# Optimization experiments

Hardware: AMD Instinct MI355X
Metric: run time of the kernel (lower is better)

## Reference

```python
import jax, jax.numpy as jnp
import numpy as np
from jax import lax

B, T, D = 2, 512, 64   # batch, temporal length, input_dim
H = 64                 # hidden_dims
OUT = 64               # output_dim
REL = 2 * D            # relation_dim = input_dim * 2 (until=True: max & min interval pooling)


def _interval_pool(f, op):
    """f: [B,T,D] -> r: [B,T,T,D] with r[:, i, j] = op-reduction of f[:, i..j] for i <= j.
    Entries with i > j are filled with f[:, i] (degenerate interval); they are never
    read because the downstream backward pooling only reduces over j >= i."""
    Tn = f.shape[1]
    idx = jnp.arange(Tn)

    def step(col, j):
        # col[:, i] holds reduce(f[:, i..j-1]) for i <= j-1, and f[:, i] otherwise
        new = op(col, f[:, j][:, None, :])                      # extend interval to j
        new = jnp.where((idx <= j)[None, :, None], new, f)      # reset i > j rows
        return new, new

    _, cols = lax.scan(step, f, jnp.arange(Tn))  # [T(j), B, T(i), D]
    return jnp.transpose(cols, (1, 2, 0, 3))     # [B, T(i), T(j), D]


def _backward_max_pool(s):
    """s: [B,T,T,C] -> out[:, i] = max_{j >= i} s[:, i, j]  (the 'broadcast' backward pool)."""
    Tn = s.shape[1]
    mask = jnp.arange(Tn)[:, None] <= jnp.arange(Tn)[None, :]   # i <= j
    neg = jnp.asarray(-1e9, s.dtype)
    return jnp.max(jnp.where(mask[None, :, :, None], s, neg), axis=2)


def setup_inputs() -> dict:
    key = jax.random.key(0)
    ks = jax.random.split(key, 7)
    f = jax.random.normal(ks[0], (B, T, D), dtype=jnp.float32)
    # step_linears per __init__: current_dim starts at REL, then hidden_dims
    dims = [(REL + REL, H), (H + REL, H), (H + REL, OUT)]
    params = {}
    for i, (din, dout) in enumerate(dims):
        params[f"W{i}"] = jax.random.normal(ks[1 + 2 * i], (din, dout), jnp.float32) / np.sqrt(din)
        params[f"b{i}"] = jnp.zeros((dout,), jnp.float32)
    return {"f": f, **params}


def reference(f, W0, b0, W1, b1, W2, b2):
    Tn = f.shape[1]
    # until=True: concat max- and min-interval pooling -> [B,T,T,2D]
    r = jnp.concatenate([_interval_pool(f, jnp.maximum),
                         _interval_pool(f, jnp.minimum)], axis=-1)
    current = r[:, :, Tn - 1]  # [B, T, REL] : reductions over suffix intervals [i, T-1]
    for W, b in ((W0, b0), (W1, b1), (W2, b2)):
        # jactorch.add_dim(current, 1, t): broadcast current (indexed by j) over new i axis
        bcast = jnp.broadcast_to(current[:, None, :, :],
                                 (f.shape[0], Tn, Tn, current.shape[-1]))
        li = jnp.concatenate([bcast, r], axis=-1)                 # [B,T,T,C+REL]
        h = jax.nn.sigmoid(jnp.einsum('bijc,co->bijo', li, W) + b)  # MLPLogic, no hidden layers
        current = _backward_max_pool(h)                           # [B,T,out]
    return current
```

## Files before the change

kernel.cpp:

```cpp
#include <hip/hip_runtime.h>
#include <hip/hip_bf16.h>
#include <math.h>

#define B_ 2
#define T_ 512
#define D_ 64
#define NBLK_PER_B 1088

typedef __attribute__((ext_vector_type(8))) short bf16x8;
typedef __attribute__((ext_vector_type(8))) unsigned short u16x8;
typedef __attribute__((ext_vector_type(4))) float f32x4;

static __device__ __forceinline__ unsigned short f2bf(float v) {
    __hip_bfloat16 h = __float2bfloat16(v);
    return *reinterpret_cast<unsigned short*>(&h);
}
static __device__ __forceinline__ float bf2f(unsigned short u) {
    return __uint_as_float(((unsigned)u) << 16);
}
static __device__ __forceinline__ unsigned short maxbits(unsigned short a, unsigned short b) {
    float m = fmaxf(bf2f(a), bf2f(b));
    return (unsigned short)(__float_as_uint(m) >> 16);
}
static __device__ __forceinline__ unsigned short minbits(unsigned short a, unsigned short b) {
    float m = fminf(bf2f(a), bf2f(b));
    return (unsigned short)(__float_as_uint(m) >> 16);
}

__global__ __launch_bounds__(512) void prep_kernel(
    const float* __restrict__ f,
    const float* __restrict__ W0, const float* __restrict__ W1, const float* __restrict__ W2,
    unsigned short* __restrict__ tmax, unsigned short* __restrict__ tmin,
    unsigned short* __restrict__ wf,
    unsigned short* __restrict__ cur0bf, unsigned short* __restrict__ intra,
    float* __restrict__ z0, float* __restrict__ z1, float* __restrict__ z2) {

    __shared__ unsigned short lmax[512][16];
    __shared__ unsigned short lmin[512][16];

    const int blk = blockIdx.x;
    const int tid = threadIdx.x;

    if (blk < 8) {
        const int b = blk & 1;
        const int c0 = (blk >> 1) * 16;
        const int t = tid;

        u16x8 mx[2], mn[2];
#pragma unroll
        for (int h = 0; h < 2; ++h) {
            const float* fp = &f[((size_t)(b * T_ + t) << 6) + c0 + h * 8];
#pragma unroll
            for (int e = 0; e < 8; ++e) {
                unsigned short u = f2bf(fp[e]);
                mx[h][e] = u; mn[h][e] = u;
            }
            size_t base = ((size_t)(b * T_ + t) << 6) + c0 + h * 8;
            *reinterpret_cast<u16x8*>(&tmax[base]) = mx[h];
            *reinterpret_cast<u16x8*>(&tmin[base]) = mn[h];
        }
        for (int k = 1; k <= 9; ++k) {
            *reinterpret_cast<u16x8*>(&lmax[t][0]) = mx[0];
            *reinterpret_cast<u16x8*>(&lmax[t][8]) = mx[1];
            *reinterpret_cast<u16x8*>(&lmin[t][0]) = mn[0];
            *reinterpret_cast<u16x8*>(&lmin[t][8]) = mn[1];
            __syncthreads();
            int t2 = t + (1 << (k - 1));
            if (t2 > T_ - 1) t2 = T_ - 1;
            u16x8 qx0 = *reinterpret_cast<const u16x8*>(&lmax[t2][0]);
            u16x8 qx1 = *reinterpret_cast<const u16x8*>(&lmax[t2][8]);
            u16x8 qn0 = *reinterpret_cast<const u16x8*>(&lmin[t2][0]);
            u16x8 qn1 = *reinterpret_cast<const u16x8*>(&lmin[t2][8]);
#pragma unroll
            for (int e = 0; e < 8; ++e) {
                mx[0][e] = maxbits(mx[0][e], qx0[e]);
                mx[1][e] = maxbits(mx[1][e], qx1[e]);
                mn[0][e] = minbits(mn[0][e], qn0[e]);
                mn[1][e] = minbits(mn[1][e], qn1[e]);
            }
            size_t base = ((size_t)((k * B_ + b) * T_ + t) << 6) + c0;
            *reinterpret_cast<u16x8*>(&tmax[base]) = mx[0];
            *reinterpret_cast<u16x8*>(&tmax[base + 8]) = mx[1];
            *reinterpret_cast<u16x8*>(&tmin[base]) = mn[0];
            *reinterpret_cast<u16x8*>(&tmin[base + 8]) = mn[1];
            __syncthreads();
        }
    } else if (blk < 11) {
        const int layer = blk - 8;
        const float* W = (layer == 0) ? W0 : ((layer == 1) ? W1 : W2);
        const int FRS = (layer == 0) ? 32 : 24;
        const int l = tid & 63;
        for (int fr = tid >> 6; fr < FRS; fr += 8) {
            int kt = fr >> 2, nt = fr & 3;
#pragma unroll
            for (int e = 0; e < 8; ++e) {
                int row = kt * 32 + ((l >> 4) << 3) + e;
                int col = nt * 16 + (l & 15);
                wf[((size_t)(layer * 32 + fr) * 64 + l) * 8 + e] = f2bf(W[row * 64 + col]);
            }
        }
    } else if (blk < 139) {
        const int x = blk - 11;
        const int c = x & 63, b = x >> 6;
        const int t = tid;
        float* smax = reinterpret_cast<float*>(lmax);
        float* smin = reinterpret_cast<float*>(lmin);
        float v = f[((size_t)(b * T_ + t) << 6) + c];
        smax[t] = v; smin[t] = v;
        __syncthreads();
        for (int off = 1; off < 512; off <<= 1) {
            float a = (t + off < 512) ? smax[t + off] : -1e30f;
            float m = (t + off < 512) ? smin[t + off] : 1e30f;
            __syncthreads();
            smax[t] = fmaxf(smax[t], a);
            smin[t] = fminf(smin[t], m);
            __syncthreads();
        }
        cur0bf[((size_t)(b * T_ + t) << 7) + c] = f2bf(smax[t]);
        cur0bf[((size_t)(b * T_ + t) << 7) + 64 + c] = f2bf(smin[t]);
    } else if (blk < 171) {
        const int x = blk - 139;
        const int jt = x & 15, b = x >> 4;
        const int jj = tid >> 4, c8 = tid & 15;
        const bool ismin = c8 >= 8;
        unsigned short (*sc)[128] = reinterpret_cast<unsigned short (*)[128]>(lmax);

        const float* fp = &f[((size_t)(b * T_ + jt * 32 + jj) << 6) + (c8 & 7) * 8];
        u16x8 r;
#pragma unroll
        for (int e = 0; e < 8; ++e) r[e] = f2bf(fp[e]);

#pragma unroll
        for (int off = 1; off < 32; off <<= 1) {
            *reinterpret_cast<u16x8*>(&sc[jj][c8 * 8]) = r;
            __syncthreads();
            if (jj >= off) {
                u16x8 q = *reinterpret_cast<const u16x8*>(&sc[jj - off][c8 * 8]);
#pragma unroll
                for (int e = 0; e < 8; ++e)
                    r[e] = ismin ? minbits(r[e], q[e]) : maxbits(r[e], q[e]);
            }
            __syncthreads();
        }
        *reinterpret_cast<u16x8*>(&intra[((size_t)((b * 16 + jt) * 32 + jj) << 7) + c8 * 8]) = r;
    } else {
        int fi = (blk - 171) * 512 + tid;
        float4 z = {0.f, 0.f, 0.f, 0.f};
        if (fi < 16384)       reinterpret_cast<float4*>(z0)[fi] = z;
        else if (fi < 32768)  reinterpret_cast<float4*>(z1)[fi - 16384] = z;
        else                  reinterpret_cast<float4*>(z2)[fi - 32768] = z;
    }
}

template <int C, bool FROM_TAB>
__global__ __launch_bounds__(256) void pair_kernel(
    const unsigned short* __restrict__ tabmax,
    const unsigned short* __restrict__ tabmin,
    const unsigned short* __restrict__ cur0bf,
    const unsigned short* __restrict__ intra,
    const float* __restrict__ curprev,
    const unsigned short* __restrict__ wf,
    const float* __restrict__ bias,
    float* __restrict__ out) {

    constexpr int KTC = C / 32;
    constexpr int KT = KTC + 4;
    constexpr int CP = (C == 128) ? 136 : 72;

    int m = blockIdx.x;
    int b = 0;
    if (m >= NBLK_PER_B) { b = 1; m -= NBLK_PER_B; }
    int jt = 0;
    while (m >= 4 * (jt + 1) * (jt + 2)) ++jt;
    const int it = m - 4 * jt * (jt + 1);
    const bool diag = (it >= 8 * jt);
    const int i0 = it * 4, j0 = jt * 32;

    const int tid = threadIdx.x;
    const int l = tid & 63, w = tid >> 6;
    const int lg = l >> 4, li = l & 15;

    __shared__ unsigned short curl[32][CP];
    __shared__ unsigned short intr[32][136];
    __shared__ unsigned short pref[4][136];

    if (FROM_TAB) {
#pragma unroll
        for (int q = 0; q < 2; ++q) {
            int chn = q * 256 + tid;
            int jj = chn >> 4, c8 = chn & 15;
            u16x8 v = *reinterpret_cast<const u16x8*>(
                &cur0bf[((size_t)(b * T_ + j0 + jj) << 7) + c8 * 8]);
            *reinterpret_cast<u16x8*>(&curl[jj][c8 * 8]) = v;
        }
    } else {
        int jj = tid >> 3, c8 = tid & 7;
        const float* cp = &curprev[((size_t)(b * T_ + j0 + jj) << 6) + c8 * 8];
        float4 v0 = *reinterpret_cast<const float4*>(cp);
        float4 v1 = *reinterpret_cast<const float4*>(cp + 4);
        u16x8 r;
        r[0] = f2bf(v0.x); r[1] = f2bf(v0.y); r[2] = f2bf(v0.z); r[3] = f2bf(v0.w);
        r[4] = f2bf(v1.x); r[5] = f2bf(v1.y); r[6] = f2bf(v1.z); r[7] = f2bf(v1.w);
        *reinterpret_cast<u16x8*>(&curl[jj][c8 * 8]) = r;
    }

    if (!diag) {
#pragma unroll
        for (int q = 0; q < 2; ++q) {
            int chn = q * 256 + tid;
            int jj = chn >> 4, c8 = chn & 15;
            u16x8 v = *reinterpret_cast<const u16x8*>(
                &intra[((size_t)((b * 16 + jt) * 32 + jj) << 7) + c8 * 8]);
            *reinterpret_cast<u16x8*>(&intr[jj][c8 * 8]) = v;
        }
        if (tid < 64) {
            int isel = tid >> 4, c8 = tid & 15;
            int i = i0 + isel;
            int len = j0 - i;
            int kk = 31 - __clz(len);
            int t2 = j0 - (1 << kk);
            const unsigned short* tab = (c8 < 8) ? tabmax : tabmin;
            int cc = (c8 & 7) * 8;
            u16x8 va = *reinterpret_cast<const u16x8*>(&tab[(((size_t)(kk * B_ + b) * T_ + i) << 6) + cc]);
            u16x8 vb = *reinterpret_cast<const u16x8*>(&tab[(((size_t)(kk * B_ + b) * T_ + t2) << 6) + cc]);
            u16x8 r;
#pragma unroll
            for (int e = 0; e < 8; ++e)
                r[e] = (c8 < 8) ? maxbits(va[e], vb[e]) : minbits(va[e], vb[e]);
            *reinterpret_cast<u16x8*>(&pref[isel][c8 * 8]) = r;
        }
    }
    __syncthreads();

    f32x4 acc[2][4];
#pragma unroll
    for (int s = 0; s < 2; ++s)
#pragma unroll
        for (int nt = 0; nt < 4; ++nt) acc[s][nt] = (f32x4){0.f, 0.f, 0.f, 0.f};

    const int pi = i0 + w;

#pragma unroll
    for (int kt = 0; kt < KT; ++kt) {
        bf16x8 bfr[4];
#pragma unroll
        for (int nt = 0; nt < 4; ++nt)
            bfr[nt] = *reinterpret_cast<const bf16x8*>(&wf[(size_t)((kt * 4 + nt) * 64 + l) * 8]);

#pragma unroll
        for (int s = 0; s < 2; ++s) {
            const int pjj = 16 * s + li;
            bf16x8 av;
            if (kt < KTC) {
                av = *reinterpret_cast<const bf16x8*>(&curl[pjj][kt * 32 + lg * 8]);
            } else {
                const int krt = kt - KTC;
                const int c8 = krt * 4 + lg;
                if (!diag) {
                    u16x8 iv = *reinterpret_cast<const u16x8*>(&intr[pjj][c8 * 8]);
                    u16x8 pv = *reinterpret_cast<const u16x8*>(&pref[w][c8 * 8]);
#pragma unroll
                    for (int e = 0; e < 8; ++e)
                        av[e] = (short)((c8 < 8) ? maxbits(iv[e], pv[e]) : minbits(iv[e], pv[e]));
                } else {
                    const int pj = j0 + pjj;
                    const int je = (pj < pi) ? pi : pj;
                    const int len = je - pi + 1;
                    const int kk = 31 - __clz(len);
                    const int t2 = je + 1 - (1 << kk);
                    const unsigned short* tab = (c8 < 8) ? tabmax : tabmin;
                    const int cc = (c8 & 7) * 8;
                    u16x8 va = *reinterpret_cast<const u16x8*>(&tab[(((size_t)(kk * B_ + b) * T_ + pi) << 6) + cc]);
                    u16x8 vb = *reinterpret_cast<const u16x8*>(&tab[(((size_t)(kk * B_ + b) * T_ + t2) << 6) + cc]);
#pragma unroll
                    for (int e = 0; e < 8; ++e)
                        av[e] = (short)((c8 < 8) ? maxbits(va[e], vb[e]) : minbits(va[e], vb[e]));
                }
            }
#pragma unroll
            for (int nt = 0; nt < 4; ++nt)
                acc[s][nt] = __builtin_amdgcn_mfma_f32_16x16x32_bf16(av, bfr[nt], acc[s][nt], 0, 0, 0);
        }
    }

#pragma unroll
    for (int nt = 0; nt < 4; ++nt) {
        float vm = -1e9f;
#pragma unroll
        for (int s = 0; s < 2; ++s)
#pragma unroll
            for (int r = 0; r < 4; ++r) {
                int jj = 16 * s + lg * 4 + r;
                if (j0 + jj >= pi) vm = fmaxf(vm, acc[s][nt][r]);
            }
        vm = fmaxf(vm, __shfl_xor(vm, 16));
        vm = fmaxf(vm, __shfl_xor(vm, 32));
        if (l < 16) {
            int o = nt * 16 + li;
            float h = 1.0f / (1.0f + __expf(-(vm + bias[o])));
            atomicMax((int*)out + (((size_t)(b * T_ + pi) << 6) + o), __float_as_int(h));
        }
    }
}

extern "C" void kernel_launch(void* const* d_in, const int* in_sizes, int n_in,
                              void* d_out, int out_size, void* d_ws, size_t ws_size,
                              hipStream_t stream) {
    const float* f  = (const float*)d_in[0];
    const float* W0 = (const float*)d_in[1];
    const float* b0 = (const float*)d_in[2];
    const float* W1 = (const float*)d_in[3];
    const float* b1 = (const float*)d_in[4];
    const float* W2 = (const float*)d_in[5];
    const float* b2 = (const float*)d_in[6];
    float* outp = (float*)d_out;

    unsigned short* tabmax = (unsigned short*)d_ws;
    unsigned short* tabmin = tabmax + 10 * B_ * T_ * 64;
    unsigned short* wf     = tabmin + 10 * B_ * T_ * 64;
    unsigned short* cur0bf = wf + 3 * 32 * 64 * 8;
    unsigned short* intra  = cur0bf + B_ * T_ * 128;
    float* cur1 = (float*)(intra + B_ * 16 * 32 * 128);
    float* cur2 = cur1 + B_ * T_ * 64;

    prep_kernel<<<dim3(267), dim3(512), 0, stream>>>(f, W0, W1, W2,
                                                     tabmax, tabmin, wf,
                                                     cur0bf, intra,
                                                     cur1, cur2, outp);

    const dim3 pgrid(B_ * NBLK_PER_B);
    pair_kernel<128, true ><<<pgrid, dim3(256), 0, stream>>>(tabmax, tabmin, cur0bf, intra,
                                                             nullptr, wf + 0 * 32 * 64 * 8, b0, cur1);
    pair_kernel<64,  false><<<pgrid, dim3(256), 0, stream>>>(tabmax, tabmin, cur0bf, intra,
                                                             cur1, wf + 1 * 32 * 64 * 8, b1, cur2);
    pair_kernel<64,  false><<<pgrid, dim3(256), 0, stream>>>(tabmax, tabmin, cur0bf, intra,
                                                             cur2, wf + 2 * 32 * 64 * 8, b2, outp);
}
```

Baseline: 83.53 us.

## Make pair blocks persistent over j-tiles with register-held weights and double-buffered staging

Each pair_kernel block now owns one 4-row i tile and walks half of its j tiles (split by parity), instead of launching one block per (i,j) tile pair. This cuts the grid from 2176 to 512 blocks. Weight fragments are loaded into registers once per block, and the per-tile inputs (cur, intra, prefix) are double-buffered in shared memory, with the next tile's global loads issued before the current tile's MFMAs. The row max is accumulated in registers across tiles, so each block issues far fewer atomics. In exchange, register pressure rises under launch_bounds(256,2), the work per block is uneven across i tiles, and there is less parallelism to hide latency.

```diff
diff --git a/kernel.cpp b/kernel.cpp
--- a/kernel.cpp
+++ b/kernel.cpp
@@ -5,7 +5,6 @@
 #define B_ 2
 #define T_ 512
 #define D_ 64
-#define NBLK_PER_B 1088
 
 typedef __attribute__((ext_vector_type(8))) short bf16x8;
 typedef __attribute__((ext_vector_type(8))) unsigned short u16x8;
@@ -153,7 +152,7 @@
 }
 
 template <int C, bool FROM_TAB>
-__global__ __launch_bounds__(256) void pair_kernel(
+__global__ __launch_bounds__(256, 2) void pair_kernel(
     const unsigned short* __restrict__ tabmax,
     const unsigned short* __restrict__ tabmin,
     const unsigned short* __restrict__ cur0bf,
@@ -167,138 +166,215 @@
     constexpr int KT = KTC + 4;
     constexpr int CP = (C == 128) ? 136 : 72;
 
-    int m = blockIdx.x;
-    int b = 0;
-    if (m >= NBLK_PER_B) { b = 1; m -= NBLK_PER_B; }
-    int jt = 0;
-    while (m >= 4 * (jt + 1) * (jt + 2)) ++jt;
-    const int it = m - 4 * jt * (jt + 1);
-    const bool diag = (it >= 8 * jt);
-    const int i0 = it * 4, j0 = jt * 32;
+    const int bx = blockIdx.x;
+    const int b = bx >> 8;
+    const int rem = bx & 255;
+    const int it = rem >> 1;
+    const int h = rem & 1;
+    const int i0 = it * 4;
+    const int jt0 = it >> 3;
+    const int start = jt0 + (h ? 1 : 2);
+    if (h && start > 15) return;
 
     const int tid = threadIdx.x;
     const int l = tid & 63, w = tid >> 6;
     const int lg = l >> 4, li = l & 15;
-
-    __shared__ unsigned short curl[32][CP];
-    __shared__ unsigned short intr[32][136];
-    __shared__ unsigned short pref[4][136];
-
-    if (FROM_TAB) {
-#pragma unroll
-        for (int q = 0; q < 2; ++q) {
-            int chn = q * 256 + tid;
-            int jj = chn >> 4, c8 = chn & 15;
-            u16x8 v = *reinterpret_cast<const u16x8*>(
-                &cur0bf[((size_t)(b * T_ + j0 + jj) << 7) + c8 * 8]);
-            *reinterpret_cast<u16x8*>(&curl[jj][c8 * 8]) = v;
+    const int pi = i0 + w;
+    const int jj_lo = tid >> 4, c8s = tid & 15;
+
+    __shared__ unsigned short curl[2][32][CP];
+    __shared__ unsigned short intr[2][32][136];
+    __shared__ unsigned short pref[2][4][136];
+
+    bf16x8 wfr[KT][4];
+#pragma unroll
+    for (int kt = 0; kt < KT; ++kt)
+#pragma unroll
+        for (int nt = 0; nt < 4; ++nt)
+            wfr[kt][nt] = *reinterpret_cast<const bf16x8*>(&wf[(size_t)((kt * 4 + nt) * 64 + l) * 8]);
+
+    float vmax[4] = {-1e9f, -1e9f, -1e9f, -1e9f};
+
+    u16x8 Rcur0, Rcur1;
+    float4 Rf0, Rf1;
+    u16x8 Rint0, Rint1;
+    u16x8 Rpva, Rpvb;
+
+    auto issue = [&](int jtn) {
+        const int j0n = jtn * 32;
+        if (FROM_TAB) {
+            const unsigned short* cb = &cur0bf[((size_t)(b * T_ + j0n) << 7)];
+            Rcur0 = *reinterpret_cast<const u16x8*>(&cb[(jj_lo << 7) + c8s * 8]);
+            Rcur1 = *reinterpret_cast<const u16x8*>(&cb[((jj_lo + 16) << 7) + c8s * 8]);
+        } else {
+            const float* cp = &curprev[((size_t)(b * T_ + j0n + (tid >> 3)) << 6) + (tid & 7) * 8];
+            Rf0 = *reinterpret_cast<const float4*>(cp);
+            Rf1 = *reinterpret_cast<const float4*>(cp + 4);
+        }
+        const unsigned short* ib = &intra[((size_t)((b * 16 + jtn) * 32) << 7)];
+        Rint0 = *reinterpret_cast<const u16x8*>(&ib[(jj_lo << 7) + c8s * 8]);
+        Rint1 = *reinterpret_cast<const u16x8*>(&ib[((jj_lo + 16) << 7) + c8s * 8]);
+        if (l < 16) {
+            int len = j0n - pi;
+            int kk = 31 - __clz(len);
+            int t2 = j0n - (1 << kk);
+            const unsigned short* tab = (li < 8) ? tabmax : tabmin;
+            int cc = (li & 7) * 8;
+            Rpva = *reinterpret_cast<const u16x8*>(&tab[(((size_t)(kk * B_ + b) * T_ + pi) << 6) + cc]);
+            Rpvb = *reinterpret_cast<const u16x8*>(&tab[(((size_t)(kk * B_ + b) * T_ + t2) << 6) + cc]);
+        }
+    };
+
+    auto wstage = [&](int p) {
+        if (FROM_TAB) {
+            *reinterpret_cast<u16x8*>(&curl[p][jj_lo][c8s * 8]) = Rcur0;
+            *reinterpret_cast<u16x8*>(&curl[p][jj_lo + 16][c8s * 8]) = Rcur1;
+        } else {
+            u16x8 r;
+            r[0] = f2bf(Rf0.x); r[1] = f2bf(Rf0.y); r[2] = f2bf(Rf0.z); r[3] = f2bf(Rf0.w);
+            r[4] = f2bf(Rf1.x); r[5] = f2bf(Rf1.y); r[6] = f2bf(Rf1.z); r[7] = f2bf(Rf1.w);
+            *reinterpret_cast<u16x8*>(&curl[p][tid >> 3][(tid & 7) * 8]) = r;
+        }
+        *reinterpret_cast<u16x8*>(&intr[p][jj_lo][c8s * 8]) = Rint0;
+        *reinterpret_cast<u16x8*>(&intr[p][jj_lo + 16][c8s * 8]) = Rint1;
+        if (l < 16) {
+            u16x8 r;
+#pragma unroll
+            for (int e = 0; e < 8; ++e)
+                r[e] = (li < 8) ? maxbits(Rpva[e], Rpvb[e]) : minbits(Rpva[e], Rpvb[e]);
+            *reinterpret_cast<u16x8*>(&pref[p][w][li * 8]) = r;
+        }
+    };
+
+    auto compute = [&](int p) {
+        f32x4 acc[2][4];
+#pragma unroll
+        for (int s = 0; s < 2; ++s)
+#pragma unroll
+            for (int nt = 0; nt < 4; ++nt) acc[s][nt] = (f32x4){0.f, 0.f, 0.f, 0.f};
+
+        u16x8 pv[4];
+#pragma unroll
+        for (int krt = 0; krt < 4; ++krt)
+            pv[krt] = *reinterpret_cast<const u16x8*>(&pref[p][w][(krt * 4 + lg) * 8]);
+
+#pragma unroll
+        for (int kt = 0; kt < KT; ++kt) {
+#pragma unroll
+            for (int s = 0; s < 2; ++s) {
+                const int pjj = 16 * s + li;
+                bf16x8 av;
+                if (kt < KTC) {
+                    av = *reinterpret_cast<const bf16x8*>(&curl[p][pjj][kt * 32 + lg * 8]);
+                } else {
+                    const int krt = kt - KTC;
+                    u16x8 iv = *reinterpret_cast<const u16x8*>(&intr[p][pjj][(krt * 4 + lg) * 8]);
+                    if (krt < 2) {
+#pragma unroll
+                        for (int e = 0; e < 8; ++e) av[e] = (short)maxbits(iv[e], pv[krt][e]);
+                    } else {
+#pragma unroll
+                        for (int e = 0; e < 8; ++e) av[e] = (short)minbits(iv[e], pv[krt][e]);
+                    }
+                }
+#pragma unroll
+                for (int nt = 0; nt < 4; ++nt)
+                    acc[s][nt] = __builtin_amdgcn_mfma_f32_16x16x32_bf16(av, wfr[kt][nt], acc[s][nt], 0, 0, 0);
+            }
+        }
+#pragma unroll
+        for (int nt = 0; nt < 4; ++nt)
+#pragma unroll
+            for (int s = 0; s < 2; ++s)
+#pragma unroll
+                for (int r = 0; r < 4; ++r)
+                    vmax[nt] = fmaxf(vmax[nt], acc[s][nt][r]);
+    };
+
+    if (!h) {
+        if (start <= 15) issue(start);
+        {
+            const int j0 = jt0 * 32;
+            f32x4 acc[2][4];
+#pragma unroll
+            for (int s = 0; s < 2; ++s)
+#pragma unroll
+                for (int nt = 0; nt < 4; ++nt) acc[s][nt] = (f32x4){0.f, 0.f, 0.f, 0.f};
+
+#pragma unroll
+            for (int kt = 0; kt < KT; ++kt) {
+#pragma unroll
+                for (int s = 0; s < 2; ++s) {
+                    const int pjj = 16 * s + li;
+                    bf16x8 av;
+                    if (kt < KTC) {
+                        if (FROM_TAB) {
+                            av = *reinterpret_cast<const bf16x8*>(
+                                &cur0bf[((size_t)(b * T_ + j0 + pjj) << 7) + kt * 32 + lg * 8]);
+                        } else {
+                            const float* cp = &curprev[((size_t)(b * T_ + j0 + pjj) << 6) + kt * 32 + lg * 8];
+                            float4 v0 = *reinterpret_cast<const float4*>(cp);
+                            float4 v1 = *reinterpret_cast<const float4*>(cp + 4);
+                            av[0] = f2bf(v0.x); av[1] = f2bf(v0.y); av[2] = f2bf(v0.z); av[3] = f2bf(v0.w);
+                            av[4] = f2bf(v1.x); av[5] = f2bf(v1.y); av[6] = f2bf(v1.z); av[7] = f2bf(v1.w);
+                        }
+                    } else {
+                        const int krt = kt - KTC;
+                        const int c8 = krt * 4 + lg;
+                        const int pj = j0 + pjj;
+                        const int je = (pj < pi) ? pi : pj;
+                        const int len = je - pi + 1;
+                        const int kk = 31 - __clz(len);
+                        const int t2 = je + 1 - (1 << kk);
+                        const unsigned short* tab = (krt < 2) ? tabmax : tabmin;
+                        const int cc = (c8 & 7) * 8;
+                        u16x8 va = *reinterpret_cast<const u16x8*>(&tab[(((size_t)(kk * B_ + b) * T_ + pi) << 6) + cc]);
+                        u16x8 vb = *reinterpret_cast<const u16x8*>(&tab[(((size_t)(kk * B_ + b) * T_ + t2) << 6) + cc]);
+                        if (krt < 2) {
+#pragma unroll
+                            for (int e = 0; e < 8; ++e) av[e] = (short)maxbits(va[e], vb[e]);
+                        } else {
+#pragma unroll
+                            for (int e = 0; e < 8; ++e) av[e] = (short)minbits(va[e], vb[e]);
+                        }
+                    }
+#pragma unroll
+                    for (int nt = 0; nt < 4; ++nt)
+                        acc[s][nt] = __builtin_amdgcn_mfma_f32_16x16x32_bf16(av, wfr[kt][nt], acc[s][nt], 0, 0, 0);
+                }
+            }
+#pragma unroll
+            for (int nt = 0; nt < 4; ++nt)
+#pragma unroll
+                for (int s = 0; s < 2; ++s)
+#pragma unroll
+                    for (int r = 0; r < 4; ++r) {
+                        int jj = 16 * s + lg * 4 + r;
+                        if (j0 + jj >= pi) vmax[nt] = fmaxf(vmax[nt], acc[s][nt][r]);
+                    }
         }
     } else {
-        int jj = tid >> 3, c8 = tid & 7;
-        const float* cp = &curprev[((size_t)(b * T_ + j0 + jj) << 6) + c8 * 8];
-        float4 v0 = *reinterpret_cast<const float4*>(cp);
-        float4 v1 = *reinterpret_cast<const float4*>(cp + 4);
-        u16x8 r;
-        r[0] = f2bf(v0.x); r[1] = f2bf(v0.y); r[2] = f2bf(v0.z); r[3] = f2bf(v0.w);
-        r[4] = f2bf(v1.x); r[5] = f2bf(v1.y); r[6] = f2bf(v1.z); r[7] = f2bf(v1.w);
-        *reinterpret_cast<u16x8*>(&curl[jj][c8 * 8]) = r;
+        issue(start);
     }
 
-    if (!diag) {
-#pragma unroll
-        for (int q = 0; q < 2; ++q) {
-            int chn = q * 256 + tid;
-            int jj = chn >> 4, c8 = chn & 15;
-            u16x8 v = *reinterpret_cast<const u16x8*>(
-                &intra[((size_t)((b * 16 + jt) * 32 + jj) << 7) + c8 * 8]);
-            *reinterpret_cast<u16x8*>(&intr[jj][c8 * 8]) = v;
-        }
-        if (tid < 64) {
-            int isel = tid >> 4, c8 = tid & 15;
-            int i = i0 + isel;
-            int len = j0 - i;
-            int kk = 31 - __clz(len);
-            int t2 = j0 - (1 << kk);
-            const unsigned short* tab = (c8 < 8) ? tabmax : tabmin;
-            int cc = (c8 & 7) * 8;
-            u16x8 va = *reinterpret_cast<const u16x8*>(&tab[(((size_t)(kk * B_ + b) * T_ + i) << 6) + cc]);
-            u16x8 vb = *reinterpret_cast<const u16x8*>(&tab[(((size_t)(kk * B_ + b) * T_ + t2) << 6) + cc]);
-            u16x8 r;
-#pragma unroll
-            for (int e = 0; e < 8; ++e)
-                r[e] = (c8 < 8) ? maxbits(va[e], vb[e]) : minbits(va[e], vb[e]);
-            *reinterpret_cast<u16x8*>(&pref[isel][c8 * 8]) = r;
-        }
+    int p = 0;
+    for (int jt = start; jt <= 15; jt += 2) {
+        wstage(p);
+        __syncthreads();
+        if (jt + 2 <= 15) issue(jt + 2);
+        compute(p);
+        p ^= 1;
     }
-    __syncthreads();
-
-    f32x4 acc[2][4];
-#pragma unroll
-    for (int s = 0; s < 2; ++s)
-#pragma unroll
-        for (int nt = 0; nt < 4; ++nt) acc[s][nt] = (f32x4){0.f, 0.f, 0.f, 0.f};
-
-    const int pi = i0 + w;
-
-#pragma unroll
-    for (int kt = 0; kt < KT; ++kt) {
-        bf16x8 bfr[4];
-#pragma unroll
-        for (int nt = 0; nt < 4; ++nt)
-            bfr[nt] = *reinterpret_cast<const bf16x8*>(&wf[(size_t)((kt * 4 + nt) * 64 + l) * 8]);
-
-#pragma unroll
-        for (int s = 0; s < 2; ++s) {
-            const int pjj = 16 * s + li;
-            bf16x8 av;
-            if (kt < KTC) {
-                av = *reinterpret_cast<const bf16x8*>(&curl[pjj][kt * 32 + lg * 8]);
-            } else {
-                const int krt = kt - KTC;
-                const int c8 = krt * 4 + lg;
-                if (!diag) {
-                    u16x8 iv = *reinterpret_cast<const u16x8*>(&intr[pjj][c8 * 8]);
-                    u16x8 pv = *reinterpret_cast<const u16x8*>(&pref[w][c8 * 8]);
-#pragma unroll
-                    for (int e = 0; e < 8; ++e)
-                        av[e] = (short)((c8 < 8) ? maxbits(iv[e], pv[e]) : minbits(iv[e], pv[e]));
-                } else {
-                    const int pj = j0 + pjj;
-                    const int je = (pj < pi) ? pi : pj;
-                    const int len = je - pi + 1;
-                    const int kk = 31 - __clz(len);
-                    const int t2 = je + 1 - (1 << kk);
-                    const unsigned short* tab = (c8 < 8) ? tabmax : tabmin;
-                    const int cc = (c8 & 7) * 8;
-                    u16x8 va = *reinterpret_cast<const u16x8*>(&tab[(((size_t)(kk * B_ + b) * T_ + pi) << 6) + cc]);
-                    u16x8 vb = *reinterpret_cast<const u16x8*>(&tab[(((size_t)(kk * B_ + b) * T_ + t2) << 6) + cc]);
-#pragma unroll
-                    for (int e = 0; e < 8; ++e)
-                        av[e] = (short)((c8 < 8) ? maxbits(va[e], vb[e]) : minbits(va[e], vb[e]));
-                }
-            }
-#pragma unroll
-            for (int nt = 0; nt < 4; ++nt)
-                acc[s][nt] = __builtin_amdgcn_mfma_f32_16x16x32_bf16(av, bfr[nt], acc[s][nt], 0, 0, 0);
-        }
-    }
 
 #pragma unroll
     for (int nt = 0; nt < 4; ++nt) {
-        float vm = -1e9f;
-#pragma unroll
-        for (int s = 0; s < 2; ++s)
-#pragma unroll
-            for (int r = 0; r < 4; ++r) {
-                int jj = 16 * s + lg * 4 + r;
-                if (j0 + jj >= pi) vm = fmaxf(vm, acc[s][nt][r]);
-            }
+        float vm = vmax[nt];
         vm = fmaxf(vm, __shfl_xor(vm, 16));
         vm = fmaxf(vm, __shfl_xor(vm, 32));
         if (l < 16) {
             int o = nt * 16 + li;
-            float h = 1.0f / (1.0f + __expf(-(vm + bias[o])));
-            atomicMax((int*)out + (((size_t)(b * T_ + pi) << 6) + o), __float_as_int(h));
+            float hh = 1.0f / (1.0f + __expf(-(vm + bias[o])));
+            atomicMax((int*)out + (((size_t)(b * T_ + pi) << 6) + o), __float_as_int(hh));
         }
     }
 }
@@ -328,7 +404,7 @@
                                                      cur0bf, intra,
                                                      cur1, cur2, outp);
 
-    const dim3 pgrid(B_ * NBLK_PER_B);
+    const dim3 pgrid(B_ * 128 * 2);
     pair_kernel<128, true ><<<pgrid, dim3(256), 0, stream>>>(tabmax, tabmin, cur0bf, intra,
                                                              nullptr, wf + 0 * 32 * 64 * 8, b0, cur1);
     pair_kernel<64,  false><<<pgrid, dim3(256), 0, stream>>>(tabmax, tabmin, cur0bf, intra,
```

Result: slower. 97.91 us (+17.2%).

## Load pair-kernel operands directly from global memory, dropping LDS staging and barrier

Applied to the files above, without the earlier changes.

Removes the shared-memory staging of the current-feature tile, the intra-block table and the prefix rows, along with the block-wide __syncthreads. Each wave now reads its MFMA A-operands straight from global memory (the L2/L1 caches) and computes its own prefix vectors in registers. It also hoists the per-lane sparse-table indices for diagonal tiles out of the k loop and resolves the max/min choice at compile time. The cost is redundant global loads across the 4 waves, since each row is now fetched once per wave, plus extra register pressure from the pv array.

```diff
diff --git a/kernel.cpp b/kernel.cpp
--- a/kernel.cpp
+++ b/kernel.cpp
@@ -165,7 +165,6 @@
 
     constexpr int KTC = C / 32;
     constexpr int KT = KTC + 4;
-    constexpr int CP = (C == 128) ? 136 : 72;
 
     int m = blockIdx.x;
     int b = 0;
@@ -179,107 +178,97 @@
     const int tid = threadIdx.x;
     const int l = tid & 63, w = tid >> 6;
     const int lg = l >> 4, li = l & 15;
-
-    __shared__ unsigned short curl[32][CP];
-    __shared__ unsigned short intr[32][136];
-    __shared__ unsigned short pref[4][136];
-
-    if (FROM_TAB) {
-#pragma unroll
-        for (int q = 0; q < 2; ++q) {
-            int chn = q * 256 + tid;
-            int jj = chn >> 4, c8 = chn & 15;
-            u16x8 v = *reinterpret_cast<const u16x8*>(
-                &cur0bf[((size_t)(b * T_ + j0 + jj) << 7) + c8 * 8]);
-            *reinterpret_cast<u16x8*>(&curl[jj][c8 * 8]) = v;
+    const int pi = i0 + w;
+
+    u16x8 pv[4];
+    int kk_s[2], t2_s[2], je_s[2];
+    if (!diag) {
+        const int len = j0 - pi;
+        const int kk = 31 - __clz(len);
+        const int t2 = j0 - (1 << kk);
+#pragma unroll
+        for (int krt = 0; krt < 4; ++krt) {
+            const int c8 = krt * 4 + lg;
+            const unsigned short* tab = (c8 < 8) ? tabmax : tabmin;
+            const int cc = (c8 & 7) * 8;
+            u16x8 va = *reinterpret_cast<const u16x8*>(&tab[(((size_t)(kk * B_ + b) * T_ + pi) << 6) + cc]);
+            u16x8 vb = *reinterpret_cast<const u16x8*>(&tab[(((size_t)(kk * B_ + b) * T_ + t2) << 6) + cc]);
+#pragma unroll
+            for (int e = 0; e < 8; ++e)
+                pv[krt][e] = (c8 < 8) ? maxbits(va[e], vb[e]) : minbits(va[e], vb[e]);
         }
     } else {
-        int jj = tid >> 3, c8 = tid & 7;
-        const float* cp = &curprev[((size_t)(b * T_ + j0 + jj) << 6) + c8 * 8];
-        float4 v0 = *reinterpret_cast<const float4*>(cp);
-        float4 v1 = *reinterpret_cast<const float4*>(cp + 4);
-        u16x8 r;
-        r[0] = f2bf(v0.x); r[1] = f2bf(v0.y); r[2] = f2bf(v0.z); r[3] = f2bf(v0.w);
-        r[4] = f2bf(v1.x); r[5] = f2bf(v1.y); r[6] = f2bf(v1.z); r[7] = f2bf(v1.w);
-        *reinterpret_cast<u16x8*>(&curl[jj][c8 * 8]) = r;
+#pragma unroll
+        for (int s = 0; s < 2; ++s) {
+            const int pj = j0 + 16 * s + li;
+            const int je = (pj < pi) ? pi : pj;
+            const int len = je - pi + 1;
+            kk_s[s] = 31 - __clz(len);
+            t2_s[s] = je + 1 - (1 << kk_s[s]);
+            je_s[s] = je;
+        }
     }
 
-    if (!diag) {
-#pragma unroll
-        for (int q = 0; q < 2; ++q) {
-            int chn = q * 256 + tid;
-            int jj = chn >> 4, c8 = chn & 15;
-            u16x8 v = *reinterpret_cast<const u16x8*>(
-                &intra[((size_t)((b * 16 + jt) * 32 + jj) << 7) + c8 * 8]);
-            *reinterpret_cast<u16x8*>(&intr[jj][c8 * 8]) = v;
-        }
-        if (tid < 64) {
-            int isel = tid >> 4, c8 = tid & 15;
-            int i = i0 + isel;
-            int len = j0 - i;
-            int kk = 31 - __clz(len);
-            int t2 = j0 - (1 << kk);
-            const unsigned short* tab = (c8 < 8) ? tabmax : tabmin;
-            int cc = (c8 & 7) * 8;
-            u16x8 va = *reinterpret_cast<const u16x8*>(&tab[(((size_t)(kk * B_ + b) * T_ + i) << 6) + cc]);
-            u16x8 vb = *reinterpret_cast<const u16x8*>(&tab[(((size_t)(kk * B_ + b) * T_ + t2) << 6) + cc]);
-            u16x8 r;
-#pragma unroll
-            for (int e = 0; e < 8; ++e)
-                r[e] = (c8 < 8) ? maxbits(va[e], vb[e]) : minbits(va[e], vb[e]);
-            *reinterpret_cast<u16x8*>(&pref[isel][c8 * 8]) = r;
-        }
-    }
-    __syncthreads();
-
     f32x4 acc[2][4];
 #pragma unroll
     for (int s = 0; s < 2; ++s)
 #pragma unroll
         for (int nt = 0; nt < 4; ++nt) acc[s][nt] = (f32x4){0.f, 0.f, 0.f, 0.f};
 
-    const int pi = i0 + w;
-
 #pragma unroll
     for (int kt = 0; kt < KT; ++kt) {
-        bf16x8 bfr[4];
+        bf16x8 wfr[4];
 #pragma unroll
         for (int nt = 0; nt < 4; ++nt)
-            bfr[nt] = *reinterpret_cast<const bf16x8*>(&wf[(size_t)((kt * 4 + nt) * 64 + l) * 8]);
+            wfr[nt] = *reinterpret_cast<const bf16x8*>(&wf[(size_t)((kt * 4 + nt) * 64 + l) * 8]);
 
 #pragma unroll
         for (int s = 0; s < 2; ++s) {
             const int pjj = 16 * s + li;
+            const int pj = j0 + pjj;
             bf16x8 av;
             if (kt < KTC) {
-                av = *reinterpret_cast<const bf16x8*>(&curl[pjj][kt * 32 + lg * 8]);
+                if (FROM_TAB) {
+                    av = *reinterpret_cast<const bf16x8*>(
+                        &cur0bf[((size_t)(b * T_ + pj) << 7) + kt * 32 + lg * 8]);
+                } else {
+                    const float* cp = &curprev[((size_t)(b * T_ + pj) << 6) + kt * 32 + lg * 8];
+                    float4 v0 = *reinterpret_cast<const float4*>(cp);
+                    float4 v1 = *reinterpret_cast<const float4*>(cp + 4);
+                    av[0] = f2bf(v0.x); av[1] = f2bf(v0.y); av[2] = f2bf(v0.z); av[3] = f2bf(v0.w);
+                    av[4] = f2bf(v1.x); av[5] = f2bf(v1.y); av[6] = f2bf(v1.z); av[7] = f2bf(v1.w);
+                }
             } else {
                 const int krt = kt - KTC;
-                const int c8 = krt * 4 + lg;
                 if (!diag) {
-                    u16x8 iv = *reinterpret_cast<const u16x8*>(&intr[pjj][c8 * 8]);
-                    u16x8 pv = *reinterpret_cast<const u16x8*>(&pref[w][c8 * 8]);
-#pragma unroll
-                    for (int e = 0; e < 8; ++e)
-                        av[e] = (short)((c8 < 8) ? maxbits(iv[e], pv[e]) : minbits(iv[e], pv[e]));
+                    u16x8 iv = *reinterpret_cast<const u16x8*>(
+                        &intra[((size_t)((b * 16 + jt) * 32 + pjj) << 7) + (krt * 4 + lg) * 8]);
+                    if (krt < 2) {
+#pragma unroll
+                        for (int e = 0; e < 8; ++e) av[e] = (short)maxbits(iv[e], pv[krt][e]);
+                    } else {
+#pragma unroll
+                        for (int e = 0; e < 8; ++e) av[e] = (short)minbits(iv[e], pv[krt][e]);
+                    }
                 } else {
-                    const int pj = j0 + pjj;
-                    const int je = (pj < pi) ? pi : pj;
-                    const int len = je - pi + 1;
-                    const int kk = 31 - __clz(len);
-                    const int t2 = je + 1 - (1 << kk);
-                    const unsigned short* tab = (c8 < 8) ? tabmax : tabmin;
+                    const int c8 = krt * 4 + lg;
+                    const unsigned short* tab = (krt < 2) ? tabmax : tabmin;
                     const int cc = (c8 & 7) * 8;
+                    const int kk = kk_s[s], t2 = t2_s[s];
                     u16x8 va = *reinterpret_cast<const u16x8*>(&tab[(((size_t)(kk * B_ + b) * T_ + pi) << 6) + cc]);
                     u16x8 vb = *reinterpret_cast<const u16x8*>(&tab[(((size_t)(kk * B_ + b) * T_ + t2) << 6) + cc]);
-#pragma unroll
-                    for (int e = 0; e < 8; ++e)
-                        av[e] = (short)((c8 < 8) ? maxbits(va[e], vb[e]) : minbits(va[e], vb[e]));
+                    if (krt < 2) {
+#pragma unroll
+                        for (int e = 0; e < 8; ++e) av[e] = (short)maxbits(va[e], vb[e]);
+                    } else {
+#pragma unroll
+                        for (int e = 0; e < 8; ++e) av[e] = (short)minbits(va[e], vb[e]);
+                    }
                 }
             }
 #pragma unroll
             for (int nt = 0; nt < 4; ++nt)
-                acc[s][nt] = __builtin_amdgcn_mfma_f32_16x16x32_bf16(av, bfr[nt], acc[s][nt], 0, 0, 0);
+                acc[s][nt] = __builtin_amdgcn_mfma_f32_16x16x32_bf16(av, wfr[nt], acc[s][nt], 0, 0, 0);
         }
     }
 
@@ -291,7 +280,7 @@
 #pragma unroll
             for (int r = 0; r < 4; ++r) {
                 int jj = 16 * s + lg * 4 + r;
-                if (j0 + jj >= pi) vm = fmaxf(vm, acc[s][nt][r]);
+                if (!diag || (j0 + jj >= pi)) vm = fmaxf(vm, acc[s][nt][r]);
             }
         vm = fmaxf(vm, __shfl_xor(vm, 16));
         vm = fmaxf(vm, __shfl_xor(vm, 32));
```

Result: slower. 124.1 us (+48.5%).

## Process eight query rows per block and reuse the current-state GEMM across them

Applied to the files above, without the earlier changes.

Each pair_kernel block now handles 8 i-rows instead of 4, halving the grid. The current-state part of the GEMM does not depend on i, so it is computed once and copied into two accumulator sets. Each wave then runs only the relation part separately for rows A and B, which reuses weight fragments and shared-memory tiles. Off-diagonal tiles also skip the j>=i masking, and launch bounds now request 4 blocks per CU. The trade-off is higher register pressure from doubled accumulators and fewer blocks available for parallelism.

```diff
diff --git a/kernel.cpp b/kernel.cpp
--- a/kernel.cpp
+++ b/kernel.cpp
@@ -5,7 +5,7 @@
 #define B_ 2
 #define T_ 512
 #define D_ 64
-#define NBLK_PER_B 1088
+#define NBLK8_PER_B 544
 
 typedef __attribute__((ext_vector_type(8))) short bf16x8;
 typedef __attribute__((ext_vector_type(8))) unsigned short u16x8;
@@ -153,7 +153,7 @@
 }
 
 template <int C, bool FROM_TAB>
-__global__ __launch_bounds__(256) void pair_kernel(
+__global__ __launch_bounds__(256, 4) void pair_kernel(
     const unsigned short* __restrict__ tabmax,
     const unsigned short* __restrict__ tabmin,
     const unsigned short* __restrict__ cur0bf,
@@ -164,25 +164,25 @@
     float* __restrict__ out) {
 
     constexpr int KTC = C / 32;
-    constexpr int KT = KTC + 4;
     constexpr int CP = (C == 128) ? 136 : 72;
 
     int m = blockIdx.x;
     int b = 0;
-    if (m >= NBLK_PER_B) { b = 1; m -= NBLK_PER_B; }
+    if (m >= NBLK8_PER_B) { b = 1; m -= NBLK8_PER_B; }
     int jt = 0;
-    while (m >= 4 * (jt + 1) * (jt + 2)) ++jt;
-    const int it = m - 4 * jt * (jt + 1);
-    const bool diag = (it >= 8 * jt);
-    const int i0 = it * 4, j0 = jt * 32;
+    while (m >= 2 * (jt + 1) * (jt + 2)) ++jt;
+    const int it = m - 2 * jt * (jt + 1);
+    const bool diag = (it >= 4 * jt);
+    const int i0 = it * 8, j0 = jt * 32;
 
     const int tid = threadIdx.x;
     const int l = tid & 63, w = tid >> 6;
     const int lg = l >> 4, li = l & 15;
+    const int piA = i0 + w, piB = i0 + 4 + w;
 
     __shared__ unsigned short curl[32][CP];
     __shared__ unsigned short intr[32][136];
-    __shared__ unsigned short pref[4][136];
+    __shared__ unsigned short pref[8][136];
 
     if (FROM_TAB) {
 #pragma unroll
@@ -213,7 +213,7 @@
                 &intra[((size_t)((b * 16 + jt) * 32 + jj) << 7) + c8 * 8]);
             *reinterpret_cast<u16x8*>(&intr[jj][c8 * 8]) = v;
         }
-        if (tid < 64) {
+        if (tid < 128) {
             int isel = tid >> 4, c8 = tid & 15;
             int i = i0 + isel;
             int len = j0 - i;
@@ -232,73 +232,132 @@
     }
     __syncthreads();
 
-    f32x4 acc[2][4];
+    int kkA[2], t2A[2], kkB[2], t2B[2];
+    if (diag) {
+#pragma unroll
+        for (int s = 0; s < 2; ++s) {
+            int pj = j0 + 16 * s + li;
+            int jeA = (pj < piA) ? piA : pj;
+            int lenA = jeA - piA + 1;
+            kkA[s] = 31 - __clz(lenA);
+            t2A[s] = jeA + 1 - (1 << kkA[s]);
+            int jeB = (pj < piB) ? piB : pj;
+            int lenB = jeB - piB + 1;
+            kkB[s] = 31 - __clz(lenB);
+            t2B[s] = jeB + 1 - (1 << kkB[s]);
+        }
+    }
+
+    f32x4 accA[2][4];
 #pragma unroll
     for (int s = 0; s < 2; ++s)
 #pragma unroll
-        for (int nt = 0; nt < 4; ++nt) acc[s][nt] = (f32x4){0.f, 0.f, 0.f, 0.f};
-
-    const int pi = i0 + w;
-
-#pragma unroll
-    for (int kt = 0; kt < KT; ++kt) {
-        bf16x8 bfr[4];
+        for (int nt = 0; nt < 4; ++nt) accA[s][nt] = (f32x4){0.f, 0.f, 0.f, 0.f};
+
+#pragma unroll
+    for (int kt = 0; kt < KTC; ++kt) {
+        bf16x8 wfr[4];
 #pragma unroll
         for (int nt = 0; nt < 4; ++nt)
-            bfr[nt] = *reinterpret_cast<const bf16x8*>(&wf[(size_t)((kt * 4 + nt) * 64 + l) * 8]);
-
+            wfr[nt] = *reinterpret_cast<const bf16x8*>(&wf[(size_t)((kt * 4 + nt) * 64 + l) * 8]);
 #pragma unroll
         for (int s = 0; s < 2; ++s) {
-            const int pjj = 16 * s + li;
-            bf16x8 av;
-            if (kt < KTC) {
-                av = *reinterpret_cast<const bf16x8*>(&curl[pjj][kt * 32 + lg * 8]);
+            bf16x8 av = *reinterpret_cast<const bf16x8*>(&curl[16 * s + li][kt * 32 + lg * 8]);
+#pragma unroll
+            for (int nt = 0; nt < 4; ++nt)
+                accA[s][nt] = __builtin_amdgcn_mfma_f32_16x16x32_bf16(av, wfr[nt], accA[s][nt], 0, 0, 0);
+        }
+    }
+
+    f32x4 accB[2][4];
+#pragma unroll
+    for (int s = 0; s < 2; ++s)
+#pragma unroll
+        for (int nt = 0; nt < 4; ++nt) accB[s][nt] = accA[s][nt];
+
+#pragma unroll
+    for (int krt = 0; krt < 4; ++krt) {
+        bf16x8 wfr[4];
+#pragma unroll
+        for (int nt = 0; nt < 4; ++nt)
+            wfr[nt] = *reinterpret_cast<const bf16x8*>(&wf[(size_t)(((KTC + krt) * 4 + nt) * 64 + l) * 8]);
+
+        u16x8 pvA, pvB;
+        if (!diag) {
+            pvA = *reinterpret_cast<const u16x8*>(&pref[w][(krt * 4 + lg) * 8]);
+            pvB = *reinterpret_cast<const u16x8*>(&pref[w + 4][(krt * 4 + lg) * 8]);
+        }
+
+#pragma unroll
+        for (int s = 0; s < 2; ++s) {
+            bf16x8 avA, avB;
+            if (!diag) {
+                u16x8 iv = *reinterpret_cast<const u16x8*>(&intr[16 * s + li][(krt * 4 + lg) * 8]);
+                if (krt < 2) {
+#pragma unroll
+                    for (int e = 0; e < 8; ++e) {
+                        avA[e] = (short)maxbits(iv[e], pvA[e]);
+                        avB[e] = (short)maxbits(iv[e], pvB[e]);
+                    }
+                } else {
+#pragma unroll
+                    for (int e = 0; e < 8; ++e) {
+                        avA[e] = (short)minbits(iv[e], pvA[e]);
+                        avB[e] = (short)minbits(iv[e], pvB[e]);
+                    }
+                }
             } else {
-                const int krt = kt - KTC;
                 const int c8 = krt * 4 + lg;
-                if (!diag) {
-                    u16x8 iv = *reinterpret_cast<const u16x8*>(&intr[pjj][c8 * 8]);
-                    u16x8 pv = *reinterpret_cast<const u16x8*>(&pref[w][c8 * 8]);
-#pragma unroll
-                    for (int e = 0; e < 8; ++e)
-                        av[e] = (short)((c8 < 8) ? maxbits(iv[e], pv[e]) : minbits(iv[e], pv[e]));
+                const unsigned short* tab = (krt < 2) ? tabmax : tabmin;
+                const int cc = (c8 & 7) * 8;
+                u16x8 vaA = *reinterpret_cast<const u16x8*>(&tab[(((size_t)(kkA[s] * B_ + b) * T_ + piA) << 6) + cc]);
+                u16x8 vbA = *reinterpret_cast<const u16x8*>(&tab[(((size_t)(kkA[s] * B_ + b) * T_ + t2A[s]) << 6) + cc]);
+                u16x8 vaB = *reinterpret_cast<const u16x8*>(&tab[(((size_t)(kkB[s] * B_ + b) * T_ + piB) << 6) + cc]);
+                u16x8 vbB = *reinterpret_cast<const u16x8*>(&tab[(((size_t)(kkB[s] * B_ + b) * T_ + t2B[s]) << 6) + cc]);
+                if (krt < 2) {
+#pragma unroll
+                    for (int e = 0; e < 8; ++e) {
+                        avA[e] = (short)maxbits(vaA[e], vbA[e]);
+                        avB[e] = (short)maxbits(vaB[e], vbB[e]);
+                    }
                 } else {
-                    const int pj = j0 + pjj;
-                    const int je = (pj < pi) ? pi : pj;
-                    const int len = je - pi + 1;
-                    const int kk = 31 - __clz(len);
-                    const int t2 = je + 1 - (1 << kk);
-                    const unsigned short* tab = (c8 < 8) ? tabmax : tabmin;
-                    const int cc = (c8 & 7) * 8;
-                    u16x8 va = *reinterpret_cast<const u16x8*>(&tab[(((size_t)(kk * B_ + b) * T_ + pi) << 6) + cc]);
-                    u16x8 vb = *reinterpret_cast<const u16x8*>(&tab[(((size_t)(kk * B_ + b) * T_ + t2) << 6) + cc]);
-#pragma unroll
-                    for (int e = 0; e < 8; ++e)
-                        av[e] = (short)((c8 < 8) ? maxbits(va[e], vb[e]) : minbits(va[e], vb[e]));
+#pragma unroll
+                    for (int e = 0; e < 8; ++e) {
+                        avA[e] = (short)minbits(vaA[e], vbA[e]);
+                        avB[e] = (short)minbits(vaB[e], vbB[e]);
+                    }
                 }
             }
 #pragma unroll
-            for (int nt = 0; nt < 4; ++nt)
-                acc[s][nt] = __builtin_amdgcn_mfma_f32_16x16x32_bf16(av, bfr[nt], acc[s][nt], 0, 0, 0);
+            for (int nt = 0; nt < 4; ++nt) {
+                accA[s][nt] = __builtin_amdgcn_mfma_f32_16x16x32_bf16(avA, wfr[nt], accA[s][nt], 0, 0, 0);
+                accB[s][nt] = __builtin_amdgcn_mfma_f32_16x16x32_bf16(avB, wfr[nt], accB[s][nt], 0, 0, 0);
+            }
         }
     }
 
 #pragma unroll
     for (int nt = 0; nt < 4; ++nt) {
-        float vm = -1e9f;
+        float vmA = -1e9f, vmB = -1e9f;
 #pragma unroll
         for (int s = 0; s < 2; ++s)
 #pragma unroll
             for (int r = 0; r < 4; ++r) {
                 int jj = 16 * s + lg * 4 + r;
-                if (j0 + jj >= pi) vm = fmaxf(vm, acc[s][nt][r]);
-            }
-        vm = fmaxf(vm, __shfl_xor(vm, 16));
-        vm = fmaxf(vm, __shfl_xor(vm, 32));
+                if (!diag || (j0 + jj >= piA)) vmA = fmaxf(vmA, accA[s][nt][r]);
+                if (!diag || (j0 + jj >= piB)) vmB = fmaxf(vmB, accB[s][nt][r]);
+            }
+        vmA = fmaxf(vmA, __shfl_xor(vmA, 16));
+        vmA = fmaxf(vmA, __shfl_xor(vmA, 32));
+        vmB = fmaxf(vmB, __shfl_xor(vmB, 16));
+        vmB = fmaxf(vmB, __shfl_xor(vmB, 32));
         if (l < 16) {
             int o = nt * 16 + li;
-            float h = 1.0f / (1.0f + __expf(-(vm + bias[o])));
-            atomicMax((int*)out + (((size_t)(b * T_ + pi) << 6) + o), __float_as_int(h));
+            float bo = bias[o];
+            float hA = 1.0f / (1.0f + __expf(-(vmA + bo)));
+            float hB = 1.0f / (1.0f + __expf(-(vmB + bo)));
+            atomicMax((int*)out + (((size_t)(b * T_ + piA) << 6) + o), __float_as_int(hA));
+            atomicMax((int*)out + (((size_t)(b * T_ + piB) << 6) + o), __float_as_int(hB));
         }
     }
 }
@@ -328,7 +387,7 @@
                                                      cur0bf, intra,
                                                      cur1, cur2, outp);
 
-    const dim3 pgrid(B_ * NBLK_PER_B);
+    const dim3 pgrid(B_ * NBLK8_PER_B);
     pair_kernel<128, true ><<<pgrid, dim3(256), 0, stream>>>(tabmax, tabmin, cur0bf, intra,
                                                              nullptr, wf + 0 * 32 * 64 * 8, b0, cur1);
     pair_kernel<64,  false><<<pgrid, dim3(256), 0, stream>>>(tabmax, tabmin, cur0bf, intra,
```

Result: slower. 93.94 us (+12.5%).
